# Kernel tuning notes

Measured on AMD Instinct MI355X. Metric: run time of the kernel, lower is better.

The kernel has to match this reference:

```python
import jax, jax.numpy as jnp
import numpy as np
import math

H = 256; L = 4; ATOM_DIM = 100; TDIM = 128; NF = 10
B = 128; NN = 32; GS = 8
N = B * NN; E = B * NN * NN
DIS = NF * 2 * 3
DIN_E = 2 * H + 6 + DIS + 3
TWO_PI = 2.0 * math.pi

# symmetric 3x3 basis for CrystalFamily.v2m (log-lattice parameterization)
_b = np.zeros((6, 3, 3), np.float32)
_b[0, 0, 0] = 1.; _b[1, 1, 1] = 1.; _b[2, 2, 2] = 1.
_b[3, 0, 1] = _b[3, 1, 0] = 1.; _b[4, 0, 2] = _b[4, 2, 0] = 1.; _b[5, 1, 2] = _b[5, 2, 1] = 1.
BASIS = jnp.asarray(_b)


def _fwd(t, atom_types, frac_coords, lattices, G, k_mean, k_std, k_mask, k_bias,
         emb_w, emb_b, latent_w, latent_b, edge_w1, edge_b1, edge_w2, edge_b2,
         node_w1, node_b1, node_w2, node_b2, coord_w, lattice_w,
         node2graph, inv_G_permutation, group_size):
    # --- gen_edges: fully connected per graph (row-major, self-loops incl.) ---
    i = jnp.arange(NN)
    src_l = jnp.repeat(i, NN); dst_l = jnp.tile(i, NN)
    off = (jnp.arange(B) * NN)[:, None]
    src = (off + src_l[None, :]).reshape(-1)   # [E]
    dst = (off + dst_l[None, :]).reshape(-1)   # [E]
    e2g = jnp.repeat(jnp.arange(B), NN * NN)   # [E]
    # logmap frac diff
    z = TWO_PI * (frac_coords[dst] - frac_coords[src])
    frac_diff = jnp.arctan2(jnp.sin(z), jnp.cos(z)) / TWO_PI  # [E,3]
    # --- compute_frac_lattice_features ---
    y = lattices * k_std + k_mean
    y = y * k_mask + k_bias
    S = jnp.einsum('bk,kij->bij', y, BASIS)                    # [B,3,3]
    Lm = jax.vmap(jax.scipy.linalg.expm)(S)                    # v2m
    ltl = jnp.einsum('bji,bjk->bik', Lm, Lm)                   # L^T L
    ltl_f = jnp.einsum('eij,ej->ei', ltl[e2g], frac_diff)
    l_f = ltl_f / (jnp.linalg.norm(ltl_f, axis=-1, keepdims=True) + 1e-6)  # [E,3]
    # --- sinusoidal distance embedding (detached in original) ---
    freqs = TWO_PI * jnp.arange(NF, dtype=jnp.float32)
    de = (frac_diff[..., None] * freqs).reshape(E, 3 * NF)
    dis = jax.lax.stop_gradient(jnp.concatenate([jnp.sin(de), jnp.cos(de)], axis=-1))  # [E,60]
    # --- node embedding + time ---
    h = atom_types @ emb_w.T + emb_b
    half = TDIM // 2
    tf = jnp.exp(-math.log(10000.0) * jnp.arange(half, dtype=jnp.float32) / half)
    ta = t[:, None] * tf[None]
    temb = jnp.concatenate([jnp.cos(ta), jnp.sin(ta)], axis=-1)  # [B,TDIM] (cos first)
    tpa = jnp.repeat(temb, NN, axis=0)                           # repeat_interleave(num_atoms)
    h = jnp.concatenate([h, tpa], axis=-1) @ latent_w.T + latent_b
    # --- message passing layers ---
    lat_e = lattices[e2g]  # [E,6]
    deg = jax.ops.segment_sum(jnp.ones((E,), jnp.float32), src, num_segments=N)
    inv_deg = 1.0 / jnp.maximum(deg, 1.0)
    for l in range(L):
        ein = jnp.concatenate([h[src], h[dst], lat_e, dis, l_f], axis=-1)  # [E,581]
        ef = jax.nn.silu(ein @ edge_w1[l].T + edge_b1[l])
        ef = jax.nn.silu(ef @ edge_w2[l].T + edge_b2[l])
        agg = jax.ops.segment_sum(ef, src, num_segments=N) * inv_deg[:, None]  # scatter-mean
        nf = jnp.concatenate([h, agg], axis=-1)
        nf = jax.nn.silu(nf @ node_w1[l].T + node_b1[l])
        nf = jax.nn.silu(nf @ node_w2[l].T + node_b2[l])
        h = h + nf  # residual
    # --- heads ---
    graph_feat = jax.ops.segment_sum(h, node2graph, num_segments=B) / NN  # mean pool
    coord = h @ coord_w.T  # [N,3]
    # equivariant split-and-average
    x = coord.reshape(B, NN, 3)
    x = jnp.repeat(x, group_size, axis=0)                                   # [B*g,NN,3]
    x = jnp.take_along_axis(x, inv_G_permutation[:, :, None], axis=1)
    x = jnp.concatenate([x, jnp.ones((B * group_size, NN, 1), x.dtype)], axis=-1)
    zc = jnp.einsum('bni,bji->bnj', x, G)[:, :, :3]
    out_x = zc.reshape(B, group_size, NN, 3).mean(axis=1).reshape(N, 3)
    lattice_out = graph_feat @ lattice_w.T
    return out_x, lattice_out


def setup_inputs() -> dict:
    key = jax.random.key(0)
    ks = jax.random.split(key, 40)
    w = lambda k, s: jax.random.normal(k, s, jnp.float32) * 0.02
    inp = {}
    inp['t'] = jax.random.uniform(ks[0], (B,))
    inp['atom_types'] = jax.random.normal(ks[1], (N, ATOM_DIM))
    inp['frac_coords'] = jax.random.uniform(ks[2], (N, 3))
    inp['lattices'] = jax.random.normal(ks[3], (B, 6)) * 0.1
    inp['G'] = jnp.eye(4)[None] + 0.1 * jax.random.normal(ks[4], (B * GS, 4, 4))
    inp['k_mean'] = jax.random.normal(ks[5], (6,)) * 0.1
    inp['k_std'] = jnp.ones((6,))
    inp['k_mask'] = jnp.ones((6,))
    inp['k_bias'] = jnp.zeros((6,))
    inp['emb_w'] = w(ks[6], (H, ATOM_DIM)); inp['emb_b'] = jnp.zeros((H,))
    inp['latent_w'] = w(ks[7], (H, H + TDIM)); inp['latent_b'] = jnp.zeros((H,))
    inp['edge_w1'] = w(ks[8], (L, H, DIN_E)); inp['edge_b1'] = jnp.zeros((L, H))
    inp['edge_w2'] = w(ks[9], (L, H, H)); inp['edge_b2'] = jnp.zeros((L, H))
    inp['node_w1'] = w(ks[10], (L, H, 2 * H)); inp['node_b1'] = jnp.zeros((L, H))
    inp['node_w2'] = w(ks[11], (L, H, H)); inp['node_b2'] = jnp.zeros((L, H))
    inp['coord_w'] = w(ks[12], (3, H))
    inp['lattice_w'] = w(ks[13], (6, H))
    inp['num_atoms'] = jnp.full((B,), NN, jnp.int32)
    inp['node2graph'] = jnp.repeat(jnp.arange(B, dtype=jnp.int32), NN)
    pk = jax.random.split(ks[14], B * GS)
    inp['inv_G_permutation'] = jax.vmap(lambda k: jax.random.permutation(k, NN))(pk).astype(jnp.int32)
    inp['group_size'] = GS
    inp['tensor_group_size'] = jnp.full((B,), GS, jnp.int32)
    return inp


def reference(t, atom_types, frac_coords, lattices, G, k_mean, k_std, k_mask, k_bias,
              emb_w, emb_b, latent_w, latent_b, edge_w1, edge_b1, edge_w2, edge_b2,
              node_w1, node_b1, node_w2, node_b2, coord_w, lattice_w,
              num_atoms, node2graph, inv_G_permutation, group_size, tensor_group_size):
    return _fwd(t, atom_types, frac_coords, lattices, G, k_mean, k_std, k_mask, k_bias,
                emb_w, emb_b, latent_w, latent_b, edge_w1, edge_b1, edge_w2, edge_b2,
                node_w1, node_b1, node_w2, node_b2, coord_w, lattice_w,
                node2graph, inv_G_permutation, group_size)
```

## Files before the change

### kernel.cpp

```cpp
#include <hip/hip_runtime.h>
#include <math.h>

namespace {
constexpr int kH = 256;
constexpr int kL = 4;
constexpr int kAtomDim = 100;
constexpr int kB = 128;
constexpr int kNN = 32;
constexpr int kGS = 8;
constexpr int kN = kB * kNN;
constexpr int kE = kB * kNN * kNN;
constexpr int kDinE = 581;
constexpr int kKF = 96;
constexpr float kTwoPi = 6.28318530717958647692f;

typedef __bf16 bf16x8 __attribute__((ext_vector_type(8)));
typedef float  f32x4  __attribute__((ext_vector_type(4)));

__device__ __forceinline__ float fsilu(float x) {
    return x * __builtin_amdgcn_rcpf(1.0f + __expf(-x));
}

__global__ void lattice_kernel(const float* __restrict__ lattices,
                               const float* __restrict__ k_mean,
                               const float* __restrict__ k_std,
                               const float* __restrict__ k_mask,
                               const float* __restrict__ k_bias,
                               float* __restrict__ ltl) {
    int b = threadIdx.x;
    if (b >= kB) return;
    double y[6];
    for (int k = 0; k < 6; ++k) {
        double v = (double)lattices[b * 6 + k] * (double)k_std[k] + (double)k_mean[k];
        y[k] = v * (double)k_mask[k] + (double)k_bias[k];
    }
    double A[9] = { y[0], y[3], y[4],
                    y[3], y[1], y[5],
                    y[4], y[5], y[2] };
    double nrm = 0.0;
    for (int i = 0; i < 3; ++i) {
        double r = fabs(A[i*3+0]) + fabs(A[i*3+1]) + fabs(A[i*3+2]);
        nrm = fmax(nrm, r);
    }
    int s = 0;
    while (nrm > 0.25 && s < 40) { nrm *= 0.5; s++; }
    double sc = 1.0;
    for (int i = 0; i < s; ++i) sc *= 0.5;
    for (int i = 0; i < 9; ++i) A[i] *= sc;
    double T[9]    = {1,0,0, 0,1,0, 0,0,1};
    double term[9] = {1,0,0, 0,1,0, 0,0,1};
    for (int it = 1; it <= 18; ++it) {
        double nt[9];
        double inv = 1.0 / (double)it;
        for (int i = 0; i < 3; ++i)
            for (int j = 0; j < 3; ++j) {
                double acc = 0.0;
                for (int k = 0; k < 3; ++k) acc += term[i*3+k] * A[k*3+j];
                nt[i*3+j] = acc * inv;
            }
        for (int i = 0; i < 9; ++i) { term[i] = nt[i]; T[i] += nt[i]; }
    }
    for (int q = 0; q < s; ++q) {
        double nt[9];
        for (int i = 0; i < 3; ++i)
            for (int j = 0; j < 3; ++j) {
                double acc = 0.0;
                for (int k = 0; k < 3; ++k) acc += T[i*3+k] * T[k*3+j];
                nt[i*3+j] = acc;
            }
        for (int i = 0; i < 9; ++i) T[i] = nt[i];
    }
    for (int i = 0; i < 3; ++i)
        for (int k = 0; k < 3; ++k) {
            double acc = 0.0;
            for (int j = 0; j < 3; ++j) acc += T[j*3+i] * T[j*3+k];
            ltl[b*9 + i*3 + k] = (float)acc;
        }
}

__global__ void feats_bf_kernel(const float* __restrict__ frac,
                                const float* __restrict__ lattices,
                                const float* __restrict__ ltl,
                                __bf16* __restrict__ out) {
    int e = blockIdx.x * blockDim.x + threadIdx.x;
    if (e >= kE) return;
    int g = e >> 10;
    int src = (g << 5) + ((e >> 5) & 31);
    int dst = (g << 5) + (e & 31);
    float d[3];
    #pragma unroll
    for (int c = 0; c < 3; ++c) {
        float delta = frac[dst*3 + c] - frac[src*3 + c];
        d[c] = delta - rintf(delta);
    }
    __attribute__((aligned(16))) __bf16 f[kKF];
    #pragma unroll
    for (int k = 0; k < 6; ++k) f[k] = (__bf16)lattices[g*6 + k];
    #pragma unroll
    for (int c = 0; c < 3; ++c) {
        float th = d[c] * kTwoPi;
        float s1 = sinf(th), c1 = cosf(th);
        float sk = 0.0f, ck = 1.0f;
        f[6  + c*10] = (__bf16)0.0f;
        f[36 + c*10] = (__bf16)1.0f;
        #pragma unroll
        for (int fr = 1; fr < 10; ++fr) {
            float ns = sk*c1 + ck*s1;
            float nc = ck*c1 - sk*s1;
            sk = ns; ck = nc;
            f[6  + c*10 + fr] = (__bf16)sk;
            f[36 + c*10 + fr] = (__bf16)ck;
        }
    }
    float v0 = ltl[g*9+0]*d[0] + ltl[g*9+1]*d[1] + ltl[g*9+2]*d[2];
    float v1 = ltl[g*9+3]*d[0] + ltl[g*9+4]*d[1] + ltl[g*9+5]*d[2];
    float v2 = ltl[g*9+6]*d[0] + ltl[g*9+7]*d[1] + ltl[g*9+8]*d[2];
    float nr = sqrtf(v0*v0 + v1*v1 + v2*v2) + 1e-6f;
    f[66] = (__bf16)(v0/nr); f[67] = (__bf16)(v1/nr); f[68] = (__bf16)(v2/nr);
    #pragma unroll
    for (int k = 69; k < kKF; ++k) f[k] = (__bf16)0.0f;
    uint4* dstp = (uint4*)(out + (size_t)e * kKF);
    const uint4* srcp = (const uint4*)f;
    #pragma unroll
    for (int i = 0; i < kKF/8; ++i) dstp[i] = srcp[i];
}

constexpr int kW1abN = 4*512*256;
constexpr int kW1cN  = 4*256*kKF;
constexpr int kW2bN  = 4*256*256;
constexpr int kNw1N  = 4*256*512;
constexpr int kNw2N  = 4*256*256;
constexpr int kAtN   = kN*128;
constexpr int kEmbwN = 256*128;
constexpr int kLatwN = 256*384;
constexpr int kConvTotal = kW1abN + kW1cN + kW2bN + kNw1N + kNw2N + kAtN + kEmbwN + kLatwN;

__global__ void conv_all(const float* __restrict__ edge_w1, const float* __restrict__ edge_w2,
                         const float* __restrict__ node_w1, const float* __restrict__ node_w2,
                         const float* __restrict__ atom, const float* __restrict__ emb_w,
                         const float* __restrict__ latent_w,
                         __bf16* __restrict__ w1ab, __bf16* __restrict__ w1c,
                         __bf16* __restrict__ w2b, __bf16* __restrict__ nw1b,
                         __bf16* __restrict__ nw2b, __bf16* __restrict__ at_bf,
                         __bf16* __restrict__ embwb, __bf16* __restrict__ latwb) {
    int i = blockIdx.x * 256 + threadIdx.x;
    if (i < kW1abN) {
        int l = i >> 17, rem = i & 131071, r = rem >> 8, k = rem & 255;
        float v = (r < 256) ? edge_w1[((size_t)(l*256 + r))*kDinE + k]
                            : edge_w1[((size_t)(l*256 + (r-256)))*kDinE + 256 + k];
        w1ab[i] = (__bf16)v;
        return;
    }
    i -= kW1abN;
    if (i < kW1cN) {
        int l = i / (256*kKF), rem = i - l*256*kKF, n = rem / kKF, k = rem - n*kKF;
        w1c[i] = (__bf16)((k < 69) ? edge_w1[((size_t)(l*256 + n))*kDinE + 512 + k] : 0.0f);
        return;
    }
    i -= kW1cN;
    if (i < kW2bN) { w2b[i] = (__bf16)edge_w2[i]; return; }
    i -= kW2bN;
    if (i < kNw1N) { nw1b[i] = (__bf16)node_w1[i]; return; }
    i -= kNw1N;
    if (i < kNw2N) { nw2b[i] = (__bf16)node_w2[i]; return; }
    i -= kNw2N;
    if (i < kAtN) {
        int n = i >> 7, k = i & 127;
        at_bf[i] = (__bf16)((k < kAtomDim) ? atom[(size_t)n*kAtomDim + k] : 0.0f);
        return;
    }
    i -= kAtN;
    if (i < kEmbwN) {
        int n = i >> 7, k = i & 127;
        embwb[i] = (__bf16)((k < kAtomDim) ? emb_w[(size_t)n*kAtomDim + k] : 0.0f);
        return;
    }
    i -= kEmbwN;
    if (i < kLatwN) { latwb[i] = (__bf16)latent_w[i]; return; }
}

__global__ void temb_kernel(const float* __restrict__ t, __bf16* __restrict__ tecat) {
    int g = blockIdx.x;
    int tid = threadIdx.x;
    float tf = expf(-logf(10000.0f) * (float)(tid & 63) / 64.0f);
    float ta = t[g] * tf;
    float v = (tid < 64) ? cosf(ta) : sinf(ta);
    __bf16 bv = (__bf16)v;
    #pragma unroll
    for (int nl = 0; nl < kNN; ++nl)
        tecat[((size_t)(g*kNN + nl))*384 + 256 + tid] = bv;
}

template<int K, int EPI>
__global__ __launch_bounds__(256) void gemm64(
        const __bf16* __restrict__ A, int lda,
        const __bf16* __restrict__ W, int ldw,
        const float* __restrict__ bias,
        float* __restrict__ out0, float* __restrict__ out1,
        __bf16* __restrict__ outbf, int ldo,
        float* __restrict__ hmaster, __bf16* __restrict__ hcat) {
    constexpr int NC = K / 32;
    __shared__ __bf16 As[2][64*40];
    __shared__ __bf16 Bs[2][64*40];
    int tid = threadIdx.x;
    int lane = tid & 63;
    int wid = tid >> 6;
    int wm = wid >> 1, wn = wid & 1;
    int r16 = lane & 15, g4 = lane >> 4;
    int mbase = blockIdx.x * 64;
    int nbase = blockIdx.y * 64;
    int srow = tid >> 2, sseg = tid & 3;
    const __bf16* agp = A + (size_t)(mbase + srow)*lda + sseg*8;
    const __bf16* wgp = W + (size_t)(nbase + srow)*ldw + sseg*8;
    int woff = srow*40 + sseg*8;

    f32x4 acc[2][2] = {};
    uint4 ra, rb;
    ra = *(const uint4*)(agp);
    rb = *(const uint4*)(wgp);
    *(uint4*)&As[0][woff] = ra;
    *(uint4*)&Bs[0][woff] = rb;
    __syncthreads();
    for (int c = 0; c < NC; ++c) {
        int cur = c & 1;
        if (c + 1 < NC) {
            ra = *(const uint4*)(agp + (c+1)*32);
            rb = *(const uint4*)(wgp + (c+1)*32);
        }
        bf16x8 af[2], bfg[2];
        #pragma unroll
        for (int mt = 0; mt < 2; ++mt)
            af[mt] = *(const bf16x8*)&As[cur][(wm*32 + mt*16 + r16)*40 + g4*8];
        #pragma unroll
        for (int nt = 0; nt < 2; ++nt)
            bfg[nt] = *(const bf16x8*)&Bs[cur][(wn*32 + nt*16 + r16)*40 + g4*8];
        #pragma unroll
        for (int mt = 0; mt < 2; ++mt)
            #pragma unroll
            for (int nt = 0; nt < 2; ++nt)
                acc[mt][nt] = __builtin_amdgcn_mfma_f32_16x16x32_bf16(af[mt], bfg[nt], acc[mt][nt], 0, 0, 0);
        if (c + 1 < NC) {
            int nxt = cur ^ 1;
            *(uint4*)&As[nxt][woff] = ra;
            *(uint4*)&Bs[nxt][woff] = rb;
        }
        __syncthreads();
    }
    #pragma unroll
    for (int mt = 0; mt < 2; ++mt)
        #pragma unroll
        for (int nt = 0; nt < 2; ++nt) {
            int n = nbase + wn*32 + nt*16 + r16;
            #pragma unroll
            for (int r = 0; r < 4; ++r) {
                int m = mbase + wm*32 + mt*16 + g4*4 + r;
                float v = acc[mt][nt][r];
                if (EPI == 0) {
                    if (n < 256) out0[(size_t)m*256 + n] = v + bias[n];
                    else         out1[(size_t)m*256 + (n - 256)] = v;
                } else if (EPI == 2) {
                    outbf[(size_t)m*ldo + n] = (__bf16)fsilu(v + bias[n]);
                } else if (EPI == 3) {
                    float hv = hmaster[(size_t)m*256 + n] + fsilu(v + bias[n]);
                    hmaster[(size_t)m*256 + n] = hv;
                    hcat[(size_t)m*512 + n] = (__bf16)hv;
                } else if (EPI == 4) {
                    outbf[(size_t)m*ldo + n] = (__bf16)(v + bias[n]);
                } else if (EPI == 5) {
                    float hv = v + bias[n];
                    hmaster[(size_t)m*256 + n] = hv;
                    hcat[(size_t)m*512 + n] = (__bf16)hv;
                }
            }
        }
}

__global__ __launch_bounds__(256, 2) void fused_edge(
        const float* __restrict__ Sb, const float* __restrict__ Dq,
        const __bf16* __restrict__ fb, const __bf16* __restrict__ w1c,
        const __bf16* __restrict__ w2, const float* __restrict__ b2,
        __bf16* __restrict__ hcat) {
    __shared__ float  Ds[32][260];
    __shared__ float  Ss[4][260];
    __shared__ __bf16 W1s[32][112];
    __shared__ __bf16 W2s[256][40];
    __shared__ __bf16 As_[128][40];

    int tid = threadIdx.x;
    int lane = tid & 63;
    int w = tid >> 6;
    int r16 = lane & 15, g4 = lane >> 4;
    int ebase = blockIdx.x * 128;
    int graph = ebase >> 10;
    int s0 = ebase >> 5;

    int wrow = tid >> 2, wq = tid & 3;
    uint4 w1r0, w1r1, w1r2;
    uint4 w2r0, w2r1, w2r2, w2r3;

    bf16x8 fReg[2][3];
    #pragma unroll
    for (int half = 0; half < 2; ++half) {
        const __bf16* fp = fb + (size_t)(ebase + w*32 + half*16 + r16)*kKF + g4*8;
        #pragma unroll
        for (int kc = 0; kc < 3; ++kc)
            fReg[half][kc] = *(const bf16x8*)(fp + kc*32);
    }
    {
        int dl = tid >> 3, seg = tid & 7;
        const float4* src = (const float4*)(Dq + (size_t)(graph*32 + dl)*256 + seg*32);
        #pragma unroll
        for (int i = 0; i < 8; ++i)
            *(float4*)&Ds[dl][seg*32 + i*4] = src[i];
    }
    {
        int sl = tid >> 6, c4 = (tid & 63) * 4;
        *(float4*)&Ss[sl][c4] = *(const float4*)(Sb + (size_t)(s0 + sl)*256 + c4);
    }
    {
        if (tid < 128) {
            const uint4* src = (const uint4*)(w1c + (size_t)wrow*kKF + wq*24);
            w1r0 = src[0]; w1r1 = src[1]; w1r2 = src[2];
        }
        w2r0 = *(const uint4*)(w2 + (size_t)(wrow      )*256 + wq*8);
        w2r1 = *(const uint4*)(w2 + (size_t)(wrow +  64)*256 + wq*8);
        w2r2 = *(const uint4*)(w2 + (size_t)(wrow + 128)*256 + wq*8);
        w2r3 = *(const uint4*)(w2 + (size_t)(wrow + 192)*256 + wq*8);
    }
    __syncthreads();

    f32x4 acc2[2][16] = {};
    for (int nc = 0; nc < 8; ++nc) {
        __syncthreads();
        if (tid < 128) {
            *(uint4*)&W1s[wrow][wq*24]      = w1r0;
            *(uint4*)&W1s[wrow][wq*24 + 8]  = w1r1;
            *(uint4*)&W1s[wrow][wq*24 + 16] = w1r2;
        }
        *(uint4*)&W2s[wrow      ][wq*8] = w2r0;
        *(uint4*)&W2s[wrow +  64][wq*8] = w2r1;
        *(uint4*)&W2s[wrow + 128][wq*8] = w2r2;
        *(uint4*)&W2s[wrow + 192][wq*8] = w2r3;
        if (nc + 1 < 8) {
            if (tid < 128) {
                const uint4* src = (const uint4*)(w1c + (size_t)((nc+1)*32 + wrow)*kKF + wq*24);
                w1r0 = src[0]; w1r1 = src[1]; w1r2 = src[2];
            }
            w2r0 = *(const uint4*)(w2 + (size_t)(wrow      )*256 + (nc+1)*32 + wq*8);
            w2r1 = *(const uint4*)(w2 + (size_t)(wrow +  64)*256 + (nc+1)*32 + wq*8);
            w2r2 = *(const uint4*)(w2 + (size_t)(wrow + 128)*256 + (nc+1)*32 + wq*8);
            w2r3 = *(const uint4*)(w2 + (size_t)(wrow + 192)*256 + (nc+1)*32 + wq*8);
        }
        __syncthreads();

        f32x4 acc1[2][2] = {};
        #pragma unroll
        for (int kc = 0; kc < 3; ++kc) {
            bf16x8 bg0 = *(const bf16x8*)&W1s[r16][kc*32 + g4*8];
            bf16x8 bg1 = *(const bf16x8*)&W1s[16 + r16][kc*32 + g4*8];
            acc1[0][0] = __builtin_amdgcn_mfma_f32_16x16x32_bf16(fReg[0][kc], bg0, acc1[0][0], 0, 0, 0);
            acc1[0][1] = __builtin_amdgcn_mfma_f32_16x16x32_bf16(fReg[0][kc], bg1, acc1[0][1], 0, 0, 0);
            acc1[1][0] = __builtin_amdgcn_mfma_f32_16x16x32_bf16(fReg[1][kc], bg0, acc1[1][0], 0, 0, 0);
            acc1[1][1] = __builtin_amdgcn_mfma_f32_16x16x32_bf16(fReg[1][kc], bg1, acc1[1][1], 0, 0, 0);
        }
        #pragma unroll
        for (int nt = 0; nt < 2; ++nt) {
            int lc = nt*16 + r16;
            int n  = nc*32 + lc;
            float sv = Ss[w][n];
            #pragma unroll
            for (int mt = 0; mt < 2; ++mt)
                #pragma unroll
                for (int r = 0; r < 4; ++r) {
                    int dl = mt*16 + g4*4 + r;
                    float v = acc1[mt][nt][r] + sv + Ds[dl][n];
                    As_[w*32 + dl][lc] = (__bf16)fsilu(v);
                }
        }
        __syncthreads();

        bf16x8 am0 = *(const bf16x8*)&As_[w*32 + r16][g4*8];
        bf16x8 am1 = *(const bf16x8*)&As_[w*32 + 16 + r16][g4*8];
        #pragma unroll
        for (int nt = 0; nt < 16; ++nt) {
            bf16x8 bv = *(const bf16x8*)&W2s[nt*16 + r16][g4*8];
            acc2[0][nt] = __builtin_amdgcn_mfma_f32_16x16x32_bf16(am0, bv, acc2[0][nt], 0, 0, 0);
            acc2[1][nt] = __builtin_amdgcn_mfma_f32_16x16x32_bf16(am1, bv, acc2[1][nt], 0, 0, 0);
        }
    }

    const float inv32 = 1.0f / 32.0f;
    #pragma unroll
    for (int nt = 0; nt < 16; ++nt) {
        int col = nt*16 + r16;
        float bb = b2[col];
        float p = 0.f;
        #pragma unroll
        for (int r = 0; r < 4; ++r)
            p += fsilu(acc2[0][nt][r] + bb) + fsilu(acc2[1][nt][r] + bb);
        p += __shfl_xor(p, 16);
        p += __shfl_xor(p, 32);
        if (lane < 16)
            hcat[(size_t)(s0 + w)*512 + 256 + col] = (__bf16)(p * inv32);
    }
}

__global__ void coord_equiv_kernel(const float* __restrict__ h,
                                   const float* __restrict__ coord_w,
                                   const float* __restrict__ G,
                                   const int* __restrict__ invp,
                                   float* __restrict__ out_x) {
    int b = blockIdx.x;
    int tid = threadIdx.x;
    __shared__ float cd[kNN][4];
    if (tid < kNN*3) {
        int nl = tid / 3, j = tid - nl*3;
        const float* hr = h + (size_t)(b*kNN + nl)*kH;
        const float* wr = coord_w + (size_t)j*kH;
        float acc = 0.f;
        #pragma unroll 4
        for (int k = 0; k < kH; ++k) acc += hr[k]*wr[k];
        cd[nl][j] = acc;
    }
    __syncthreads();
    if (tid < kNN*3) {
        int nl = tid / 3, j = tid - nl*3;
        float acc = 0.f;
        for (int g = 0; g < kGS; ++g) {
            int bg = b*kGS + g;
            int p = invp[bg*kNN + nl];
            const float* Gr = G + (size_t)bg*16 + j*4;
            acc += cd[p][0]*Gr[0] + cd[p][1]*Gr[1] + cd[p][2]*Gr[2] + Gr[3];
        }
        out_x[(size_t)(b*kNN + nl)*3 + j] = acc * (1.0f/kGS);
    }
}

__global__ void graphfeat_kernel(const float* __restrict__ h,
                                 const float* __restrict__ lattice_w,
                                 float* __restrict__ out_lat) {
    int g = blockIdx.x;
    int c = threadIdx.x;
    __shared__ float gf[kH];
    float s = 0.f;
    for (int nl = 0; nl < kNN; ++nl) s += h[(size_t)(g*kNN + nl)*kH + c];
    gf[c] = s * (1.0f/kNN);
    __syncthreads();
    if (c < 6) {
        const float* wr = lattice_w + (size_t)c*kH;
        float acc = 0.f;
        #pragma unroll 4
        for (int k = 0; k < kH; ++k) acc += gf[k]*wr[k];
        out_lat[g*6 + c] = acc;
    }
}

}

extern "C" void kernel_launch(void* const* d_in, const int* in_sizes, int n_in,
                              void* d_out, int out_size, void* d_ws, size_t ws_size,
                              hipStream_t stream) {
    (void)in_sizes; (void)n_in; (void)out_size; (void)ws_size;
    const float* t         = (const float*)d_in[0];
    const float* atom      = (const float*)d_in[1];
    const float* frac      = (const float*)d_in[2];
    const float* lattices  = (const float*)d_in[3];
    const float* G         = (const float*)d_in[4];
    const float* k_mean    = (const float*)d_in[5];
    const float* k_std     = (const float*)d_in[6];
    const float* k_mask    = (const float*)d_in[7];
    const float* k_bias    = (const float*)d_in[8];
    const float* emb_w     = (const float*)d_in[9];
    const float* emb_b     = (const float*)d_in[10];
    const float* latent_w  = (const float*)d_in[11];
    const float* latent_b  = (const float*)d_in[12];
    const float* edge_w1   = (const float*)d_in[13];
    const float* edge_b1   = (const float*)d_in[14];
    const float* edge_w2   = (const float*)d_in[15];
    const float* edge_b2   = (const float*)d_in[16];
    const float* node_w1   = (const float*)d_in[17];
    const float* node_b1   = (const float*)d_in[18];
    const float* node_w2   = (const float*)d_in[19];
    const float* node_b2   = (const float*)d_in[20];
    const float* coord_w   = (const float*)d_in[21];
    const float* lattice_w = (const float*)d_in[22];
    const int*   invp      = (const int*)d_in[25];

    float* out_x   = (float*)d_out;
    float* out_lat = (float*)d_out + kN*3;

    char* base = (char*)d_ws;
    size_t off = 0;
    auto carve = [&](size_t bytes) { char* p = base + off; off += bytes; return p; };
    float*  ltl    = (float*)carve(8192);
    float*  h      = (float*)carve(4194304);
    float*  Sbuf   = (float*)carve(4194304);
    float*  Dbuf   = (float*)carve(4194304);
    __bf16* hcat   = (__bf16*)carve(4194304);
    __bf16* t1     = (__bf16*)carve(2097152);
    __bf16* fb     = (__bf16*)carve(25165824);
    __bf16* w1ab   = (__bf16*)carve(1048576);
    __bf16* w1c    = (__bf16*)carve(262144);
    __bf16* w2b    = (__bf16*)carve(524288);
    __bf16* nw1b   = (__bf16*)carve(1048576);
    __bf16* nw2b   = (__bf16*)carve(524288);
    __bf16* at_bf  = (__bf16*)carve(1048576);
    __bf16* embwb  = (__bf16*)carve(65536);
    __bf16* latwb  = (__bf16*)carve(196608);
    __bf16* tecat  = (__bf16*)carve(3145728);

    lattice_kernel<<<1, 128, 0, stream>>>(lattices, k_mean, k_std, k_mask, k_bias, ltl);
    feats_bf_kernel<<<kE/256, 256, 0, stream>>>(frac, lattices, ltl, fb);
    conv_all<<<(kConvTotal + 255)/256, 256, 0, stream>>>(
        edge_w1, edge_w2, node_w1, node_w2, atom, emb_w, latent_w,
        w1ab, w1c, w2b, nw1b, nw2b, at_bf, embwb, latwb);
    temb_kernel<<<kB, 128, 0, stream>>>(t, tecat);

    gemm64<128, 4><<<dim3(64, 4), 256, 0, stream>>>(
        at_bf, 128, embwb, 128, emb_b,
        nullptr, nullptr, tecat, 384, nullptr, nullptr);
    gemm64<384, 5><<<dim3(64, 4), 256, 0, stream>>>(
        tecat, 384, latwb, 384, latent_b,
        nullptr, nullptr, nullptr, 0, h, hcat);

    for (int l = 0; l < kL; ++l) {
        gemm64<256, 0><<<dim3(64, 8), 256, 0, stream>>>(
            hcat, 512, w1ab + (size_t)l*512*256, 256,
            edge_b1 + l*256, Sbuf, Dbuf, nullptr, 0, nullptr, nullptr);
        fused_edge<<<1024, 256, 0, stream>>>(
            Sbuf, Dbuf, fb, w1c + (size_t)l*256*kKF,
            w2b + (size_t)l*256*256, edge_b2 + l*256, hcat);
        gemm64<512, 2><<<dim3(64, 4), 256, 0, stream>>>(
            hcat, 512, nw1b + (size_t)l*256*512, 512,
            node_b1 + l*256, nullptr, nullptr, t1, 256, nullptr, nullptr);
        gemm64<256, 3><<<dim3(64, 4), 256, 0, stream>>>(
            t1, 256, nw2b + (size_t)l*256*256, 256,
            node_b2 + l*256, nullptr, nullptr, nullptr, 0, h, hcat);
    }
    coord_equiv_kernel<<<kB, 128, 0, stream>>>(h, coord_w, G, invp, out_x);
    graphfeat_kernel<<<kB, 256, 0, stream>>>(h, lattice_w, out_lat);
}
```

Measured before the change: 455.8 us.

## Halve fused_edge tile, store S/D in bf16, raise occupancy

The S/D projection outputs are now written and read as bf16 instead of fp32, halving their global traffic and shared memory footprint. fused_edge processes 64 edges per block instead of 128, splitting the W2 output columns across wave pairs. This shrinks accumulators from 32 to 16 tiles per wave and allows 3 blocks per CU. W1 fragments are loaded directly from global memory each chunk, replacing the register-prefetched LDS staging of W1 and W2. This drops the W2 prefetch overlap, doubles W2 reloads per edge, and adds bf16 rounding of S and D.

```diff
diff --git a/kernel.cpp b/kernel.cpp
--- a/kernel.cpp
+++ b/kernel.cpp
@@ -196,8 +196,8 @@
         const __bf16* __restrict__ A, int lda,
         const __bf16* __restrict__ W, int ldw,
         const float* __restrict__ bias,
-        float* __restrict__ out0, float* __restrict__ out1,
         __bf16* __restrict__ outbf, int ldo,
+        __bf16* __restrict__ outbf2,
         float* __restrict__ hmaster, __bf16* __restrict__ hcat) {
     constexpr int NC = K / 32;
     __shared__ __bf16 As[2][64*40];
@@ -256,8 +256,8 @@
                 int m = mbase + wm*32 + mt*16 + g4*4 + r;
                 float v = acc[mt][nt][r];
                 if (EPI == 0) {
-                    if (n < 256) out0[(size_t)m*256 + n] = v + bias[n];
-                    else         out1[(size_t)m*256 + (n - 256)] = v;
+                    if (n < 256) outbf[(size_t)m*256 + n] = (__bf16)(v + bias[n]);
+                    else         outbf2[(size_t)m*256 + (n - 256)] = (__bf16)v;
                 } else if (EPI == 2) {
                     outbf[(size_t)m*ldo + n] = (__bf16)fsilu(v + bias[n]);
                 } else if (EPI == 3) {
@@ -275,115 +275,85 @@
         }
 }
 
-__global__ __launch_bounds__(256, 2) void fused_edge(
-        const float* __restrict__ Sb, const float* __restrict__ Dq,
+__global__ __launch_bounds__(256, 3) void fused_edge(
+        const __bf16* __restrict__ Sb, const __bf16* __restrict__ Dq,
         const __bf16* __restrict__ fb, const __bf16* __restrict__ w1c,
         const __bf16* __restrict__ w2, const float* __restrict__ b2,
         __bf16* __restrict__ hcat) {
-    __shared__ float  Ds[32][260];
-    __shared__ float  Ss[4][260];
-    __shared__ __bf16 W1s[32][112];
+    __shared__ __bf16 Ds[32][264];
+    __shared__ __bf16 Ss[2][264];
     __shared__ __bf16 W2s[256][40];
-    __shared__ __bf16 As_[128][40];
+    __shared__ __bf16 As_[64][40];
 
     int tid = threadIdx.x;
     int lane = tid & 63;
     int w = tid >> 6;
+    int sl = w >> 1;
+    int ch = w & 1;
     int r16 = lane & 15, g4 = lane >> 4;
-    int ebase = blockIdx.x * 128;
+    int ebase = blockIdx.x * 64;
     int graph = ebase >> 10;
     int s0 = ebase >> 5;
 
-    int wrow = tid >> 2, wq = tid & 3;
-    uint4 w1r0, w1r1, w1r2;
-    uint4 w2r0, w2r1, w2r2, w2r3;
-
-    bf16x8 fReg[2][3];
-    #pragma unroll
-    for (int half = 0; half < 2; ++half) {
-        const __bf16* fp = fb + (size_t)(ebase + w*32 + half*16 + r16)*kKF + g4*8;
-        #pragma unroll
-        for (int kc = 0; kc < 3; ++kc)
-            fReg[half][kc] = *(const bf16x8*)(fp + kc*32);
+    bf16x8 fReg[3];
+    {
+        const __bf16* fp = fb + (size_t)(ebase + sl*32 + ch*16 + r16)*kKF + g4*8;
+        fReg[0] = *(const bf16x8*)(fp);
+        fReg[1] = *(const bf16x8*)(fp + 32);
+        fReg[2] = *(const bf16x8*)(fp + 64);
     }
     {
         int dl = tid >> 3, seg = tid & 7;
-        const float4* src = (const float4*)(Dq + (size_t)(graph*32 + dl)*256 + seg*32);
-        #pragma unroll
-        for (int i = 0; i < 8; ++i)
-            *(float4*)&Ds[dl][seg*32 + i*4] = src[i];
-    }
-    {
-        int sl = tid >> 6, c4 = (tid & 63) * 4;
-        *(float4*)&Ss[sl][c4] = *(const float4*)(Sb + (size_t)(s0 + sl)*256 + c4);
-    }
-    {
-        if (tid < 128) {
-            const uint4* src = (const uint4*)(w1c + (size_t)wrow*kKF + wq*24);
-            w1r0 = src[0]; w1r1 = src[1]; w1r2 = src[2];
-        }
-        w2r0 = *(const uint4*)(w2 + (size_t)(wrow      )*256 + wq*8);
-        w2r1 = *(const uint4*)(w2 + (size_t)(wrow +  64)*256 + wq*8);
-        w2r2 = *(const uint4*)(w2 + (size_t)(wrow + 128)*256 + wq*8);
-        w2r3 = *(const uint4*)(w2 + (size_t)(wrow + 192)*256 + wq*8);
-    }
-    __syncthreads();
-
-    f32x4 acc2[2][16] = {};
+        const uint4* src = (const uint4*)(Dq + (size_t)(graph*32 + dl)*256 + seg*32);
+        uint4* dst = (uint4*)&Ds[dl][seg*32];
+        dst[0] = src[0]; dst[1] = src[1]; dst[2] = src[2]; dst[3] = src[3];
+    }
+    if (tid < 64) {
+        int slr = tid >> 5, c8 = (tid & 31)*8;
+        *(uint4*)&Ss[slr][c8] = *(const uint4*)(Sb + (size_t)(s0 + slr)*256 + c8);
+    }
+
+    int wrow = tid >> 2, wq = tid & 3;
+    f32x4 acc2[2][8] = {};
     for (int nc = 0; nc < 8; ++nc) {
+        if (nc) __syncthreads();
+        #pragma unroll
+        for (int p = 0; p < 4; ++p)
+            *(uint4*)&W2s[wrow + p*64][wq*8] =
+                *(const uint4*)(w2 + (size_t)(wrow + p*64)*256 + nc*32 + wq*8);
+        bf16x8 bg0[3], bg1[3];
+        #pragma unroll
+        for (int kc = 0; kc < 3; ++kc) {
+            bg0[kc] = *(const bf16x8*)(w1c + (size_t)(nc*32 + r16)*kKF + kc*32 + g4*8);
+            bg1[kc] = *(const bf16x8*)(w1c + (size_t)(nc*32 + 16 + r16)*kKF + kc*32 + g4*8);
+        }
         __syncthreads();
-        if (tid < 128) {
-            *(uint4*)&W1s[wrow][wq*24]      = w1r0;
-            *(uint4*)&W1s[wrow][wq*24 + 8]  = w1r1;
-            *(uint4*)&W1s[wrow][wq*24 + 16] = w1r2;
-        }
-        *(uint4*)&W2s[wrow      ][wq*8] = w2r0;
-        *(uint4*)&W2s[wrow +  64][wq*8] = w2r1;
-        *(uint4*)&W2s[wrow + 128][wq*8] = w2r2;
-        *(uint4*)&W2s[wrow + 192][wq*8] = w2r3;
-        if (nc + 1 < 8) {
-            if (tid < 128) {
-                const uint4* src = (const uint4*)(w1c + (size_t)((nc+1)*32 + wrow)*kKF + wq*24);
-                w1r0 = src[0]; w1r1 = src[1]; w1r2 = src[2];
-            }
-            w2r0 = *(const uint4*)(w2 + (size_t)(wrow      )*256 + (nc+1)*32 + wq*8);
-            w2r1 = *(const uint4*)(w2 + (size_t)(wrow +  64)*256 + (nc+1)*32 + wq*8);
-            w2r2 = *(const uint4*)(w2 + (size_t)(wrow + 128)*256 + (nc+1)*32 + wq*8);
-            w2r3 = *(const uint4*)(w2 + (size_t)(wrow + 192)*256 + (nc+1)*32 + wq*8);
-        }
-        __syncthreads();
-
-        f32x4 acc1[2][2] = {};
+
+        f32x4 acc1[2] = {};
         #pragma unroll
         for (int kc = 0; kc < 3; ++kc) {
-            bf16x8 bg0 = *(const bf16x8*)&W1s[r16][kc*32 + g4*8];
-            bf16x8 bg1 = *(const bf16x8*)&W1s[16 + r16][kc*32 + g4*8];
-            acc1[0][0] = __builtin_amdgcn_mfma_f32_16x16x32_bf16(fReg[0][kc], bg0, acc1[0][0], 0, 0, 0);
-            acc1[0][1] = __builtin_amdgcn_mfma_f32_16x16x32_bf16(fReg[0][kc], bg1, acc1[0][1], 0, 0, 0);
-            acc1[1][0] = __builtin_amdgcn_mfma_f32_16x16x32_bf16(fReg[1][kc], bg0, acc1[1][0], 0, 0, 0);
-            acc1[1][1] = __builtin_amdgcn_mfma_f32_16x16x32_bf16(fReg[1][kc], bg1, acc1[1][1], 0, 0, 0);
+            acc1[0] = __builtin_amdgcn_mfma_f32_16x16x32_bf16(fReg[kc], bg0[kc], acc1[0], 0, 0, 0);
+            acc1[1] = __builtin_amdgcn_mfma_f32_16x16x32_bf16(fReg[kc], bg1[kc], acc1[1], 0, 0, 0);
         }
         #pragma unroll
         for (int nt = 0; nt < 2; ++nt) {
             int lc = nt*16 + r16;
             int n  = nc*32 + lc;
-            float sv = Ss[w][n];
+            float sv = (float)Ss[sl][n];
             #pragma unroll
-            for (int mt = 0; mt < 2; ++mt)
-                #pragma unroll
-                for (int r = 0; r < 4; ++r) {
-                    int dl = mt*16 + g4*4 + r;
-                    float v = acc1[mt][nt][r] + sv + Ds[dl][n];
-                    As_[w*32 + dl][lc] = (__bf16)fsilu(v);
-                }
+            for (int r = 0; r < 4; ++r) {
+                int row16 = g4*4 + r;
+                float v = acc1[nt][r] + sv + (float)Ds[ch*16 + row16][n];
+                As_[sl*32 + ch*16 + row16][lc] = (__bf16)fsilu(v);
+            }
         }
         __syncthreads();
 
-        bf16x8 am0 = *(const bf16x8*)&As_[w*32 + r16][g4*8];
-        bf16x8 am1 = *(const bf16x8*)&As_[w*32 + 16 + r16][g4*8];
-        #pragma unroll
-        for (int nt = 0; nt < 16; ++nt) {
-            bf16x8 bv = *(const bf16x8*)&W2s[nt*16 + r16][g4*8];
+        bf16x8 am0 = *(const bf16x8*)&As_[sl*32 + r16][g4*8];
+        bf16x8 am1 = *(const bf16x8*)&As_[sl*32 + 16 + r16][g4*8];
+        #pragma unroll
+        for (int nt = 0; nt < 8; ++nt) {
+            bf16x8 bv = *(const bf16x8*)&W2s[ch*128 + nt*16 + r16][g4*8];
             acc2[0][nt] = __builtin_amdgcn_mfma_f32_16x16x32_bf16(am0, bv, acc2[0][nt], 0, 0, 0);
             acc2[1][nt] = __builtin_amdgcn_mfma_f32_16x16x32_bf16(am1, bv, acc2[1][nt], 0, 0, 0);
         }
@@ -391,8 +361,8 @@
 
     const float inv32 = 1.0f / 32.0f;
     #pragma unroll
-    for (int nt = 0; nt < 16; ++nt) {
-        int col = nt*16 + r16;
+    for (int nt = 0; nt < 8; ++nt) {
+        int col = ch*128 + nt*16 + r16;
         float bb = b2[col];
         float p = 0.f;
         #pragma unroll
@@ -401,7 +371,7 @@
         p += __shfl_xor(p, 16);
         p += __shfl_xor(p, 32);
         if (lane < 16)
-            hcat[(size_t)(s0 + w)*512 + 256 + col] = (__bf16)(p * inv32);
+            hcat[(size_t)(s0 + sl)*512 + 256 + col] = (__bf16)(p * inv32);
     }
 }
 
@@ -494,8 +464,8 @@
     auto carve = [&](size_t bytes) { char* p = base + off; off += bytes; return p; };
     float*  ltl    = (float*)carve(8192);
     float*  h      = (float*)carve(4194304);
-    float*  Sbuf   = (float*)carve(4194304);
-    float*  Dbuf   = (float*)carve(4194304);
+    __bf16* Sbuf   = (__bf16*)carve(2097152);
+    __bf16* Dbuf   = (__bf16*)carve(2097152);
     __bf16* hcat   = (__bf16*)carve(4194304);
     __bf16* t1     = (__bf16*)carve(2097152);
     __bf16* fb     = (__bf16*)carve(25165824);
@@ -518,24 +488,24 @@
 
     gemm64<128, 4><<<dim3(64, 4), 256, 0, stream>>>(
         at_bf, 128, embwb, 128, emb_b,
-        nullptr, nullptr, tecat, 384, nullptr, nullptr);
+        tecat, 384, nullptr, nullptr, nullptr);
     gemm64<384, 5><<<dim3(64, 4), 256, 0, stream>>>(
         tecat, 384, latwb, 384, latent_b,
-        nullptr, nullptr, nullptr, 0, h, hcat);
+        nullptr, 0, nullptr, h, hcat);
 
     for (int l = 0; l < kL; ++l) {
         gemm64<256, 0><<<dim3(64, 8), 256, 0, stream>>>(
             hcat, 512, w1ab + (size_t)l*512*256, 256,
-            edge_b1 + l*256, Sbuf, Dbuf, nullptr, 0, nullptr, nullptr);
-        fused_edge<<<1024, 256, 0, stream>>>(
+            edge_b1 + l*256, Sbuf, 256, Dbuf, nullptr, nullptr);
+        fused_edge<<<2048, 256, 0, stream>>>(
             Sbuf, Dbuf, fb, w1c + (size_t)l*256*kKF,
             w2b + (size_t)l*256*256, edge_b2 + l*256, hcat);
         gemm64<512, 2><<<dim3(64, 4), 256, 0, stream>>>(
             hcat, 512, nw1b + (size_t)l*256*512, 512,
-            node_b1 + l*256, nullptr, nullptr, t1, 256, nullptr, nullptr);
+            node_b1 + l*256, t1, 256, nullptr, nullptr, nullptr);
         gemm64<256, 3><<<dim3(64, 4), 256, 0, stream>>>(
             t1, 256, nw2b + (size_t)l*256*256, 256,
-            node_b2 + l*256, nullptr, nullptr, nullptr, 0, h, hcat);
+            node_b2 + l*256, nullptr, 0, nullptr, h, hcat);
     }
     coord_equiv_kernel<<<kB, 128, 0, stream>>>(h, coord_w, G, invp, out_x);
     graphfeat_kernel<<<kB, 256, 0, stream>>>(h, lattice_w, out_lat);
```

Measured after the change: 456.2 us. Within noise of the previous version (+0.1%).
